# Kernel tuning notes

Hardware: AMD Instinct MI355X
Metric: run time of the kernel (lower is better)

Reference implementation:

```python
import jax, jax.numpy as jnp
import numpy as np

SEQ_LEN = 4096
D_IN = 2048
D_OUT = 2048
DROPOUT_P = 0.5


def setup_inputs() -> dict:
    key = jax.random.key(0)
    kx, kq, kk, kv = jax.random.split(key, 4)
    return {
        "x": jax.random.normal(kx, (SEQ_LEN, D_IN), dtype=jnp.float32),
        "W_query": jax.random.uniform(kq, (D_IN, D_OUT), dtype=jnp.float32),
        "W_key": jax.random.uniform(kk, (D_IN, D_OUT), dtype=jnp.float32),
        "W_value": jax.random.uniform(kv, (D_IN, D_OUT), dtype=jnp.float32),
    }


def reference(x, W_query, W_key, W_value):
    # projections: [S, d_in] @ [d_in, d_out] -> [S, d_out]
    queries = x @ W_query
    keys = x @ W_key
    values = x @ W_value
    # full score matrix [S, S]
    attn_scores = queries @ keys.T
    S = attn_scores.shape[0]
    causal_mask = jnp.triu(jnp.ones((S, S), dtype=bool), k=1)
    masked = jnp.where(causal_mask, -jnp.inf, attn_scores)
    scale = jnp.sqrt(jnp.asarray(keys.shape[-1], dtype=masked.dtype))
    attn_weights = jax.nn.softmax(masked / scale, axis=1)
    # dropout p=0.5 (train mode), inverted scaling, deterministic key
    keep = jax.random.bernoulli(jax.random.key(42), 1.0 - DROPOUT_P, attn_weights.shape)
    attn_weights = jnp.where(keep, attn_weights / (1.0 - DROPOUT_P), 0.0)
    context_vec = attn_weights @ values  # [S, d_out]
    return context_vec
```

## Files before the change

kernel.cpp:

```cpp
#include <hip/hip_runtime.h>
#include <cstdint>
#include <cstddef>
#include <cmath>

#define SEQ 4096
#define DM  2048

typedef unsigned int u32;
typedef unsigned short u16;
typedef __attribute__((ext_vector_type(8))) short bf16x8;
typedef __attribute__((ext_vector_type(4))) float f32x4;

__device__ __forceinline__ u16 f2bf(float f) {
  u32 u = __float_as_uint(f);
  return (u16)((u + 0x7FFFu + ((u >> 16) & 1u)) >> 16);
}
__device__ __forceinline__ float bf2f(u16 h) { return __uint_as_float(((u32)h) << 16); }

__device__ __forceinline__ u32 rotl32(u32 x, int r) { return (x << r) | (x >> (32 - r)); }

__device__ __forceinline__ void tf2x32(u32 c0, u32 c1, u32& o0, u32& o1) {
  const u32 k0 = 0u, k1 = 42u, k2 = 0x1BD11BDAu ^ 0u ^ 42u;
  u32 x0 = c0 + k0;
  u32 x1 = c1 + k1;
#define TFR(r) { x0 += x1; x1 = rotl32(x1, (r)); x1 ^= x0; }
  TFR(13) TFR(15) TFR(26) TFR(6)   x0 += k1; x1 += k2 + 1u;
  TFR(17) TFR(29) TFR(16) TFR(24)  x0 += k2; x1 += k0 + 2u;
  TFR(13) TFR(15) TFR(26) TFR(6)   x0 += k0; x1 += k1 + 3u;
  TFR(17) TFR(29) TFR(16) TFR(24)  x0 += k1; x1 += k2 + 4u;
  TFR(13) TFR(15) TFR(26) TFR(6)   x0 += k2; x1 += k0 + 5u;
#undef TFR
  o0 = x0; o1 = x1;
}

__device__ __forceinline__ bool dropout_keep(u32 idx) {
  u32 a, b; tf2x32(0u, idx, a, b);
  return (((a ^ b) & 0x80000000u) == 0u);
}

__device__ __forceinline__ void g2l16(const void* g, void* l) {
  __builtin_amdgcn_global_load_lds((const __attribute__((address_space(1))) u32*)g,
                                   (__attribute__((address_space(3))) u32*)l, 16, 0, 0);
}

#define MFMA16(a, b, c) __builtin_amdgcn_mfma_f32_16x16x32_bf16(a, b, c, 0, 0, 0)

template <bool SPLIT>
__device__ __forceinline__ void gemm_core(
    const u16* __restrict__ Ah, const u16* __restrict__ Al,
    const u16* __restrict__ Bh, const u16* __restrict__ Bl,
    int lda, int ldb, int rowBlock, int colBlock, int kmax,
    f32x4 (&acc)[4][4])
{
  __shared__ __align__(16) u16 Als[SPLIT ? 2 : 1][128 * 32];
  __shared__ __align__(16) u16 Bls[SPLIT ? 2 : 1][128 * 32];
  const int tid  = threadIdx.x;
  const int wid  = tid >> 6;
  const int lane = tid & 63;
  const int wr   = (wid & 1) << 6;
  const int wc   = (wid >> 1) << 6;
  const int lrow = lane & 15;
  const int lk   = (((lane >> 4) ^ ((lrow >> 1) & 3)) << 3);
  const int srow = wid * 32 + (lane >> 2);
  const int skol = (((lane & 3) ^ ((lane >> 3) & 3)) << 3);

  const f32x4 zero = {0.f, 0.f, 0.f, 0.f};
#pragma unroll
  for (int i = 0; i < 4; ++i)
#pragma unroll
    for (int j = 0; j < 4; ++j) acc[i][j] = zero;

  for (int kb = 0; kb < kmax; kb += 32) {
#pragma unroll
    for (int t = 0; t < 2; ++t) {
      const size_t ga = (size_t)(rowBlock + srow + t * 16) * lda + kb + skol;
      const size_t gb = (size_t)(colBlock + srow + t * 16) * ldb + kb + skol;
      const int lo = (wid * 32 + t * 16) * 32;
      g2l16(Ah + ga, &Als[0][lo]);
      g2l16(Bh + gb, &Bls[0][lo]);
      if constexpr (SPLIT) {
        g2l16(Al + ga, &Als[1][lo]);
        g2l16(Bl + gb, &Bls[1][lo]);
      }
    }
    __syncthreads();

    bf16x8 ah[4], bh[4], al[4], bl[4];
#pragma unroll
    for (int r = 0; r < 4; ++r) {
      ah[r] = *(const bf16x8*)&Als[0][(wr + r * 16 + lrow) * 32 + lk];
      bh[r] = *(const bf16x8*)&Bls[0][(wc + r * 16 + lrow) * 32 + lk];
      if constexpr (SPLIT) {
        al[r] = *(const bf16x8*)&Als[1][(wr + r * 16 + lrow) * 32 + lk];
        bl[r] = *(const bf16x8*)&Bls[1][(wc + r * 16 + lrow) * 32 + lk];
      }
    }
#pragma unroll
    for (int r = 0; r < 4; ++r)
#pragma unroll
      for (int c = 0; c < 4; ++c) {
        acc[r][c] = MFMA16(ah[r], bh[c], acc[r][c]);
        if constexpr (SPLIT) {
          acc[r][c] = MFMA16(ah[r], bl[c], acc[r][c]);
          acc[r][c] = MFMA16(al[r], bh[c], acc[r][c]);
        }
      }
    __syncthreads();
  }
}

__global__ __launch_bounds__(256) void k_split_x(const float* __restrict__ X,
                                                 u16* __restrict__ Xh, u16* __restrict__ Xl) {
  const size_t i = ((size_t)blockIdx.x * 256 + threadIdx.x) * 4;
  const float4 v = *(const float4*)(X + i);
  ushort4 h, l;
  h.x = f2bf(v.x); l.x = f2bf(v.x - bf2f(h.x));
  h.y = f2bf(v.y); l.y = f2bf(v.y - bf2f(h.y));
  h.z = f2bf(v.z); l.z = f2bf(v.z - bf2f(h.z));
  h.w = f2bf(v.w); l.w = f2bf(v.w - bf2f(h.w));
  *(ushort4*)(Xh + i) = h;
  *(ushort4*)(Xl + i) = l;
}

__global__ __launch_bounds__(256) void k_split_w(
    const float* __restrict__ Wq, const float* __restrict__ Wk, const float* __restrict__ Wv,
    u16* __restrict__ Wqh, u16* __restrict__ Wql,
    u16* __restrict__ Wkh, u16* __restrict__ Wkl, u16* __restrict__ Wvh) {
  const int z = blockIdx.z;
  const float* W = (z == 0) ? Wq : (z == 1) ? Wk : Wv;
  u16* Oh = (z == 0) ? Wqh : (z == 1) ? Wkh : Wvh;
  u16* Ol = (z == 0) ? Wql : Wkl;
  __shared__ float t[32][33];
  const int tx = threadIdx.x & 31, ty = threadIdx.x >> 5;
  const int n0 = blockIdx.x * 32, k0 = blockIdx.y * 32;
#pragma unroll
  for (int i = 0; i < 4; ++i)
    t[ty + i * 8][tx] = W[(size_t)(k0 + ty + i * 8) * DM + n0 + tx];
  __syncthreads();
#pragma unroll
  for (int i = 0; i < 4; ++i) {
    const int n = ty + i * 8;
    const float v = t[tx][n];
    const u16 h = f2bf(v);
    const size_t off = (size_t)(n0 + n) * DM + k0 + tx;
    Oh[off] = h;
    if (z < 2) Ol[off] = f2bf(v - bf2f(h));
  }
}

__global__ __launch_bounds__(256) void k_proj_qk(
    const u16* __restrict__ Xh, const u16* __restrict__ Xl,
    const u16* __restrict__ Wqh, const u16* __restrict__ Wql,
    const u16* __restrict__ Wkh, const u16* __restrict__ Wkl,
    u16* __restrict__ Qh, u16* __restrict__ Ql,
    u16* __restrict__ Kh, u16* __restrict__ Kl, float rscaleQ)
{
  const int z = blockIdx.z;
  const u16* Bh = z ? Wkh : Wqh;
  const u16* Bl = z ? Wkl : Wql;
  u16* Oh = z ? Kh : Qh;
  u16* Ol = z ? Kl : Ql;
  const float rs = z ? 1.0f : rscaleQ;
  f32x4 acc[4][4];
  gemm_core<true>(Xh, Xl, Bh, Bl, DM, DM, blockIdx.y * 128, blockIdx.x * 128, DM, acc);

  const int lane = threadIdx.x & 63, wid = threadIdx.x >> 6;
  const int r0 = blockIdx.y * 128 + ((wid & 1) << 6) + ((lane >> 4) << 2);
  const int c0 = blockIdx.x * 128 + ((wid >> 1) << 6) + (lane & 15);
#pragma unroll
  for (int r = 0; r < 4; ++r)
#pragma unroll
    for (int c = 0; c < 4; ++c) {
      const int col = c0 + c * 16;
#pragma unroll
      for (int e = 0; e < 4; ++e) {
        const float v = acc[r][c][e] * rs;
        const u16 h = f2bf(v);
        const size_t off = (size_t)(r0 + r * 16 + e) * DM + col;
        Oh[off] = h;
        Ol[off] = f2bf(v - bf2f(h));
      }
    }
}

__global__ __launch_bounds__(256) void k_proj_v(
    const u16* __restrict__ Xh, const u16* __restrict__ Wvh, u16* __restrict__ Vt)
{
  f32x4 acc[4][4];
  gemm_core<false>(Xh, nullptr, Wvh, nullptr, DM, DM, blockIdx.y * 128, blockIdx.x * 128, DM, acc);

  const int lane = threadIdx.x & 63, wid = threadIdx.x >> 6;
  const int r0 = blockIdx.y * 128 + ((wid & 1) << 6) + ((lane >> 4) << 2);
  const int c0 = blockIdx.x * 128 + ((wid >> 1) << 6) + (lane & 15);
#pragma unroll
  for (int r = 0; r < 4; ++r)
#pragma unroll
    for (int c = 0; c < 4; ++c) {
      const int d = c0 + c * 16;
      const int s0 = r0 + r * 16;
      ushort4 pk;
      pk.x = f2bf(acc[r][c][0]); pk.y = f2bf(acc[r][c][1]);
      pk.z = f2bf(acc[r][c][2]); pk.w = f2bf(acc[r][c][3]);
      *(ushort4*)(Vt + (size_t)d * SEQ + s0) = pk;
    }
}

__global__ __launch_bounds__(256) void k_scores(
    const u16* __restrict__ Qh, const u16* __restrict__ Ql,
    const u16* __restrict__ Kh, const u16* __restrict__ Kl, float* __restrict__ S)
{
  const int bid = blockIdx.x;
  int by = (int)((sqrtf(8.0f * (float)bid + 1.0f) - 1.0f) * 0.5f);
  while ((by + 1) * (by + 2) / 2 <= bid) ++by;
  while (by * (by + 1) / 2 > bid) --by;
  const int bx = bid - by * (by + 1) / 2;

  f32x4 acc[4][4];
  gemm_core<true>(Qh, Ql, Kh, Kl, DM, DM, by * 128, bx * 128, DM, acc);

  const int lane = threadIdx.x & 63, wid = threadIdx.x >> 6;
  const int r0 = by * 128 + ((wid & 1) << 6) + ((lane >> 4) << 2);
  const int c0 = bx * 128 + ((wid >> 1) << 6) + (lane & 15);
#pragma unroll
  for (int r = 0; r < 4; ++r)
#pragma unroll
    for (int c = 0; c < 4; ++c)
#pragma unroll
      for (int e = 0; e < 4; ++e)
        S[(size_t)(r0 + r * 16 + e) * SEQ + (c0 + c * 16)] = acc[r][c][e];
}

__global__ __launch_bounds__(256) void k_softmax_dropout(const float* __restrict__ S,
                                                         u16* __restrict__ P) {
  const int row = blockIdx.x;
  const int n = row + 1;
  const int nt = (n + 1023) >> 10;
  const int tid = threadIdx.x;
  __shared__ float buf[SEQ];
  __shared__ float red[4];
  __shared__ float bcast;
  const float* srow = S + (size_t)row * SEQ;

  float lmax = -INFINITY;
  for (int t = 0; t < nt; ++t) {
    int j4 = tid + t * 256;
    float4 v = *(const float4*)(srow + (size_t)j4 * 4);
    int b = j4 * 4;
    float x0 = (b + 0 < n) ? v.x : -INFINITY;
    float x1 = (b + 1 < n) ? v.y : -INFINITY;
    float x2 = (b + 2 < n) ? v.z : -INFINITY;
    float x3 = (b + 3 < n) ? v.w : -INFINITY;
    buf[b + 0] = x0; buf[b + 1] = x1; buf[b + 2] = x2; buf[b + 3] = x3;
    lmax = fmaxf(lmax, fmaxf(fmaxf(x0, x1), fmaxf(x2, x3)));
  }
  for (int off = 32; off > 0; off >>= 1) lmax = fmaxf(lmax, __shfl_down(lmax, off, 64));
  if ((tid & 63) == 0) red[tid >> 6] = lmax;
  __syncthreads();
  if (tid == 0) bcast = fmaxf(fmaxf(red[0], red[1]), fmaxf(red[2], red[3]));
  __syncthreads();
  const float m = bcast;

  float lsum = 0.f;
  for (int t = 0; t < nt; ++t) {
    int b = (tid + t * 256) * 4;
    float e0 = expf(buf[b + 0] - m);
    float e1 = expf(buf[b + 1] - m);
    float e2 = expf(buf[b + 2] - m);
    float e3 = expf(buf[b + 3] - m);
    buf[b + 0] = e0; buf[b + 1] = e1; buf[b + 2] = e2; buf[b + 3] = e3;
    lsum += (e0 + e1) + (e2 + e3);
  }
  for (int off = 32; off > 0; off >>= 1) lsum += __shfl_down(lsum, off, 64);
  if ((tid & 63) == 0) red[tid >> 6] = lsum;
  __syncthreads();
  if (tid == 0) bcast = (red[0] + red[1]) + (red[2] + red[3]);
  __syncthreads();
  const float total = bcast;

  u16* prow = P + (size_t)row * SEQ;
  const int zeroEnd = ((row >> 7) + 1) << 7;
  for (int j = tid; j < zeroEnd; j += 256) {
    float out = 0.f;
    if (j < n) {
      const float w = buf[j] / total;
      out = dropout_keep((u32)(row * SEQ + j)) ? w * 2.0f : 0.f;
    }
    prow[j] = f2bf(out);
  }
}

__global__ __launch_bounds__(256) void k_pv(const u16* __restrict__ P,
                                            const u16* __restrict__ Vt,
                                            float* __restrict__ O) {
  const int by = (SEQ / 128 - 1) - blockIdx.y;
  f32x4 acc[4][4];
  gemm_core<false>(P, nullptr, Vt, nullptr, SEQ, SEQ, by * 128, blockIdx.x * 128,
                   (by + 1) * 128, acc);

  const int lane = threadIdx.x & 63, wid = threadIdx.x >> 6;
  const int r0 = by * 128 + ((wid & 1) << 6) + ((lane >> 4) << 2);
  const int c0 = blockIdx.x * 128 + ((wid >> 1) << 6) + (lane & 15);
#pragma unroll
  for (int r = 0; r < 4; ++r)
#pragma unroll
    for (int c = 0; c < 4; ++c)
#pragma unroll
      for (int e = 0; e < 4; ++e)
        O[(size_t)(r0 + r * 16 + e) * DM + (c0 + c * 16)] = acc[r][c][e];
}

extern "C" void kernel_launch(void* const* d_in, const int* in_sizes, int n_in,
                              void* d_out, int out_size, void* d_ws, size_t ws_size,
                              hipStream_t stream) {
  const float* x  = (const float*)d_in[0];
  const float* Wq = (const float*)d_in[1];
  const float* Wk = (const float*)d_in[2];
  const float* Wv = (const float*)d_in[3];

  const size_t PL = (size_t)SEQ * DM;
  const size_t WL = (size_t)DM * DM;
  u16* base = (u16*)d_ws;
  u16* Qh = base;
  u16* Ql = Qh + PL;
  u16* Kh = Ql + PL;
  u16* Kl = Kh + PL;
  u16* Vt = Kl + PL;
  u16* P  = base;
  u16* regA = Vt + PL;
  u16* Xh  = regA;
  u16* Xl  = Xh + PL;
  u16* Wqh = Xl + PL;
  u16* Wql = Wqh + WL;
  u16* Wkh = Wql + WL;
  u16* Wkl = Wkh + WL;
  u16* Wvh = Wkl + WL;
  float* S = (float*)regA;

  const float rscale = 1.0f / sqrtf(2048.0f);
  dim3 blk(256);
  k_split_x<<<dim3((unsigned)(PL / 1024)), blk, 0, stream>>>(x, Xh, Xl);
  k_split_w<<<dim3(DM / 32, DM / 32, 3), blk, 0, stream>>>(Wq, Wk, Wv, Wqh, Wql, Wkh, Wkl, Wvh);
  k_proj_qk<<<dim3(DM / 128, SEQ / 128, 2), blk, 0, stream>>>(Xh, Xl, Wqh, Wql, Wkh, Wkl,
                                                              Qh, Ql, Kh, Kl, rscale);
  k_proj_v<<<dim3(DM / 128, SEQ / 128), blk, 0, stream>>>(Xh, Wvh, Vt);
  k_scores<<<dim3((SEQ / 128) * (SEQ / 128 + 1) / 2), blk, 0, stream>>>(Qh, Ql, Kh, Kl, S);
  k_softmax_dropout<<<dim3(SEQ), blk, 0, stream>>>(S, P);
  k_pv<<<dim3(DM / 128, SEQ / 128), blk, 0, stream>>>(P, Vt, (float*)d_out);
}
```

Baseline: 661.3 us.

## Store low bf16 halves in MFMA fragment order and load directly to registers

The low-order bf16 residual planes (Xl, Wql/Wkl, Ql/Kl) are now written in a pre-tiled per-lane fragment layout, so the split GEMM loads them straight from global memory into registers instead of staging them through LDS. This halves LDS traffic and shared memory per block in the Q/K projection and score GEMMs, which may raise occupancy. The split kernels and the QK projection epilogue are rewritten to emit this layout, with the epilogue using shared memory for the reshuffle. The cost is extra global loads issued before the barrier and more complex epilogues.

After: 681.5 us. +3.1%, slower.

```diff
diff --git a/kernel.cpp b/kernel.cpp
--- a/kernel.cpp
+++ b/kernel.cpp
@@ -45,15 +45,15 @@
 
 #define MFMA16(a, b, c) __builtin_amdgcn_mfma_f32_16x16x32_bf16(a, b, c, 0, 0, 0)
 
-template <bool SPLIT>
-__device__ __forceinline__ void gemm_core(
-    const u16* __restrict__ Ah, const u16* __restrict__ Al,
-    const u16* __restrict__ Bh, const u16* __restrict__ Bl,
+
+__device__ __forceinline__ void gemm_core_split(
+    const u16* __restrict__ Ah, const u16* __restrict__ AlFT,
+    const u16* __restrict__ Bh, const u16* __restrict__ BlFT,
     int lda, int ldb, int rowBlock, int colBlock, int kmax,
-    f32x4 (&acc)[4][4])
+    f32x4 (&acc)[4][4], u16* smem)
 {
-  __shared__ __align__(16) u16 Als[SPLIT ? 2 : 1][128 * 32];
-  __shared__ __align__(16) u16 Bls[SPLIT ? 2 : 1][128 * 32];
+  u16* Als = smem;
+  u16* Bls = smem + 4096;
   const int tid  = threadIdx.x;
   const int wid  = tid >> 6;
   const int lane = tid & 63;
@@ -63,6 +63,9 @@
   const int lk   = (((lane >> 4) ^ ((lrow >> 1) & 3)) << 3);
   const int srow = wid * 32 + (lane >> 2);
   const int skol = (((lane & 3) ^ ((lane >> 3) & 3)) << 3);
+  const int KA32 = lda >> 5, KB32 = ldb >> 5;
+  const int rtA = (rowBlock >> 4) + ((wid & 1) << 2);
+  const int rtB = (colBlock >> 4) + ((wid >> 1) << 2);
 
   const f32x4 zero = {0.f, 0.f, 0.f, 0.f};
 #pragma unroll
@@ -71,55 +74,113 @@
     for (int j = 0; j < 4; ++j) acc[i][j] = zero;
 
   for (int kb = 0; kb < kmax; kb += 32) {
+    const int kt = kb >> 5;
+    bf16x8 al[4], bl[4];
+#pragma unroll
+    for (int r = 0; r < 4; ++r) {
+      al[r] = *(const bf16x8*)(AlFT + (((size_t)(rtA + r) * KA32 + kt) * 64 + lane) * 8);
+      bl[r] = *(const bf16x8*)(BlFT + (((size_t)(rtB + r) * KB32 + kt) * 64 + lane) * 8);
+    }
 #pragma unroll
     for (int t = 0; t < 2; ++t) {
       const size_t ga = (size_t)(rowBlock + srow + t * 16) * lda + kb + skol;
       const size_t gb = (size_t)(colBlock + srow + t * 16) * ldb + kb + skol;
       const int lo = (wid * 32 + t * 16) * 32;
-      g2l16(Ah + ga, &Als[0][lo]);
-      g2l16(Bh + gb, &Bls[0][lo]);
-      if constexpr (SPLIT) {
-        g2l16(Al + ga, &Als[1][lo]);
-        g2l16(Bl + gb, &Bls[1][lo]);
-      }
+      g2l16(Ah + ga, &Als[lo]);
+      g2l16(Bh + gb, &Bls[lo]);
     }
     __syncthreads();
 
-    bf16x8 ah[4], bh[4], al[4], bl[4];
+    bf16x8 ah[4], bh[4];
 #pragma unroll
     for (int r = 0; r < 4; ++r) {
-      ah[r] = *(const bf16x8*)&Als[0][(wr + r * 16 + lrow) * 32 + lk];
-      bh[r] = *(const bf16x8*)&Bls[0][(wc + r * 16 + lrow) * 32 + lk];
-      if constexpr (SPLIT) {
-        al[r] = *(const bf16x8*)&Als[1][(wr + r * 16 + lrow) * 32 + lk];
-        bl[r] = *(const bf16x8*)&Bls[1][(wc + r * 16 + lrow) * 32 + lk];
-      }
+      ah[r] = *(const bf16x8*)&Als[(wr + r * 16 + lrow) * 32 + lk];
+      bh[r] = *(const bf16x8*)&Bls[(wc + r * 16 + lrow) * 32 + lk];
     }
 #pragma unroll
     for (int r = 0; r < 4; ++r)
 #pragma unroll
       for (int c = 0; c < 4; ++c) {
         acc[r][c] = MFMA16(ah[r], bh[c], acc[r][c]);
-        if constexpr (SPLIT) {
-          acc[r][c] = MFMA16(ah[r], bl[c], acc[r][c]);
-          acc[r][c] = MFMA16(al[r], bh[c], acc[r][c]);
-        }
+        acc[r][c] = MFMA16(ah[r], bl[c], acc[r][c]);
+        acc[r][c] = MFMA16(al[r], bh[c], acc[r][c]);
       }
     __syncthreads();
   }
 }
 
+__device__ __forceinline__ void gemm_core(
+    const u16* __restrict__ Ah, const u16* __restrict__ Bh,
+    int lda, int ldb, int rowBlock, int colBlock, int kmax,
+    f32x4 (&acc)[4][4])
+{
+  __shared__ __align__(16) u16 Als[128 * 32];
+  __shared__ __align__(16) u16 Bls[128 * 32];
+  const int tid  = threadIdx.x;
+  const int wid  = tid >> 6;
+  const int lane = tid & 63;
+  const int wr   = (wid & 1) << 6;
+  const int wc   = (wid >> 1) << 6;
+  const int lrow = lane & 15;
+  const int lk   = (((lane >> 4) ^ ((lrow >> 1) & 3)) << 3);
+  const int srow = wid * 32 + (lane >> 2);
+  const int skol = (((lane & 3) ^ ((lane >> 3) & 3)) << 3);
+
+  const f32x4 zero = {0.f, 0.f, 0.f, 0.f};
+#pragma unroll
+  for (int i = 0; i < 4; ++i)
+#pragma unroll
+    for (int j = 0; j < 4; ++j) acc[i][j] = zero;
+
+  for (int kb = 0; kb < kmax; kb += 32) {
+#pragma unroll
+    for (int t = 0; t < 2; ++t) {
+      const size_t ga = (size_t)(rowBlock + srow + t * 16) * lda + kb + skol;
+      const size_t gb = (size_t)(colBlock + srow + t * 16) * ldb + kb + skol;
+      const int lo = (wid * 32 + t * 16) * 32;
+      g2l16(Ah + ga, &Als[lo]);
+      g2l16(Bh + gb, &Bls[lo]);
+    }
+    __syncthreads();
+
+    bf16x8 ah[4], bh[4];
+#pragma unroll
+    for (int r = 0; r < 4; ++r) {
+      ah[r] = *(const bf16x8*)&Als[(wr + r * 16 + lrow) * 32 + lk];
+      bh[r] = *(const bf16x8*)&Bls[(wc + r * 16 + lrow) * 32 + lk];
+    }
+#pragma unroll
+    for (int r = 0; r < 4; ++r)
+#pragma unroll
+      for (int c = 0; c < 4; ++c)
+        acc[r][c] = MFMA16(ah[r], bh[c], acc[r][c]);
+    __syncthreads();
+  }
+}
+
 __global__ __launch_bounds__(256) void k_split_x(const float* __restrict__ X,
                                                  u16* __restrict__ Xh, u16* __restrict__ Xl) {
-  const size_t i = ((size_t)blockIdx.x * 256 + threadIdx.x) * 4;
-  const float4 v = *(const float4*)(X + i);
-  ushort4 h, l;
-  h.x = f2bf(v.x); l.x = f2bf(v.x - bf2f(h.x));
-  h.y = f2bf(v.y); l.y = f2bf(v.y - bf2f(h.y));
-  h.z = f2bf(v.z); l.z = f2bf(v.z - bf2f(h.z));
-  h.w = f2bf(v.w); l.w = f2bf(v.w - bf2f(h.w));
-  *(ushort4*)(Xh + i) = h;
-  *(ushort4*)(Xl + i) = l;
+  const int wid = threadIdx.x >> 6, lane = threadIdx.x & 63;
+  const int kt = blockIdx.x;
+  const int rt = blockIdx.y * 4 + wid;
+  const int row = rt * 16 + (lane & 15);
+  const int col = kt * 32 + ((lane >> 4) << 3);
+  const float* src = X + (size_t)row * DM + col;
+  const float4 v0 = *(const float4*)src;
+  const float4 v1 = *(const float4*)(src + 4);
+  float v[8] = {v0.x, v0.y, v0.z, v0.w, v1.x, v1.y, v1.z, v1.w};
+  u16 h[8], l[8];
+#pragma unroll
+  for (int j = 0; j < 8; ++j) {
+    h[j] = f2bf(v[j]);
+    l[j] = f2bf(v[j] - bf2f(h[j]));
+  }
+  u16* hp = Xh + (size_t)row * DM + col;
+  *(ushort4*)hp = *(ushort4*)&h[0];
+  *(ushort4*)(hp + 4) = *(ushort4*)&h[4];
+  u16* lp = Xl + (((size_t)rt * 64 + kt) * 64 + lane) * 8;
+  *(ushort4*)lp = *(ushort4*)&l[0];
+  *(ushort4*)(lp + 4) = *(ushort4*)&l[4];
 }
 
 __global__ __launch_bounds__(256) void k_split_w(
@@ -130,21 +191,40 @@
   const float* W = (z == 0) ? Wq : (z == 1) ? Wk : Wv;
   u16* Oh = (z == 0) ? Wqh : (z == 1) ? Wkh : Wvh;
   u16* Ol = (z == 0) ? Wql : Wkl;
-  __shared__ float t[32][33];
-  const int tx = threadIdx.x & 31, ty = threadIdx.x >> 5;
-  const int n0 = blockIdx.x * 32, k0 = blockIdx.y * 32;
-#pragma unroll
-  for (int i = 0; i < 4; ++i)
-    t[ty + i * 8][tx] = W[(size_t)(k0 + ty + i * 8) * DM + n0 + tx];
-  __syncthreads();
-#pragma unroll
-  for (int i = 0; i < 4; ++i) {
-    const int n = ty + i * 8;
-    const float v = t[tx][n];
-    const u16 h = f2bf(v);
-    const size_t off = (size_t)(n0 + n) * DM + k0 + tx;
-    Oh[off] = h;
-    if (z < 2) Ol[off] = f2bf(v - bf2f(h));
+  __shared__ float t[64][65];
+  const int tid = threadIdx.x;
+  const int n0 = blockIdx.x * 64, k0 = blockIdx.y * 64;
+  const int tx = tid & 63, ty = tid >> 6;
+#pragma unroll
+  for (int i = 0; i < 16; ++i)
+    t[ty * 16 + i][tx] = W[(size_t)(k0 + ty * 16 + i) * DM + n0 + tx];
+  __syncthreads();
+  {
+    const int nl = tid >> 2, kc = (tid & 3) * 16;
+    u16 h[16];
+#pragma unroll
+    for (int i = 0; i < 16; ++i) h[i] = f2bf(t[kc + i][nl]);
+    u16* hp = Oh + (size_t)(n0 + nl) * DM + k0 + kc;
+#pragma unroll
+    for (int i = 0; i < 4; ++i) *(ushort4*)(hp + i * 4) = *(ushort4*)&h[i * 4];
+  }
+  if (z < 2) {
+    const int wid = tid >> 6, lane = tid & 63;
+#pragma unroll
+    for (int kt = 0; kt < 2; ++kt) {
+      const int nl = wid * 16 + (lane & 15);
+      const int kc = kt * 32 + ((lane >> 4) << 3);
+      u16 l[8];
+#pragma unroll
+      for (int j = 0; j < 8; ++j) {
+        const float v = t[kc + j][nl];
+        l[j] = f2bf(v - bf2f(f2bf(v)));
+      }
+      const int rtg = (n0 >> 4) + wid, ktg = (k0 >> 5) + kt;
+      u16* lp = Ol + (((size_t)rtg * 64 + ktg) * 64 + lane) * 8;
+      *(ushort4*)lp = *(ushort4*)&l[0];
+      *(ushort4*)(lp + 4) = *(ushort4*)&l[4];
+    }
   }
 }
 
@@ -155,39 +235,53 @@
     u16* __restrict__ Qh, u16* __restrict__ Ql,
     u16* __restrict__ Kh, u16* __restrict__ Kl, float rscaleQ)
 {
+  __shared__ __align__(16) u16 smem[128 * 128];
   const int z = blockIdx.z;
   const u16* Bh = z ? Wkh : Wqh;
   const u16* Bl = z ? Wkl : Wql;
   u16* Oh = z ? Kh : Qh;
   u16* Ol = z ? Kl : Ql;
   const float rs = z ? 1.0f : rscaleQ;
+  const int rowBlock = blockIdx.y * 128, colBlock = blockIdx.x * 128;
   f32x4 acc[4][4];
-  gemm_core<true>(Xh, Xl, Bh, Bl, DM, DM, blockIdx.y * 128, blockIdx.x * 128, DM, acc);
+  gemm_core_split(Xh, Xl, Bh, Bl, DM, DM, rowBlock, colBlock, DM, acc, smem);
 
   const int lane = threadIdx.x & 63, wid = threadIdx.x >> 6;
-  const int r0 = blockIdx.y * 128 + ((wid & 1) << 6) + ((lane >> 4) << 2);
-  const int c0 = blockIdx.x * 128 + ((wid >> 1) << 6) + (lane & 15);
+  const int lr0 = ((wid & 1) << 6) + ((lane >> 4) << 2);
+  const int lc0 = ((wid >> 1) << 6) + (lane & 15);
 #pragma unroll
   for (int r = 0; r < 4; ++r)
 #pragma unroll
-    for (int c = 0; c < 4; ++c) {
-      const int col = c0 + c * 16;
+    for (int c = 0; c < 4; ++c)
 #pragma unroll
       for (int e = 0; e < 4; ++e) {
         const float v = acc[r][c][e] * rs;
         const u16 h = f2bf(v);
-        const size_t off = (size_t)(r0 + r * 16 + e) * DM + col;
-        Oh[off] = h;
-        Ol[off] = f2bf(v - bf2f(h));
+        const int lrow = lr0 + r * 16 + e, lcol = lc0 + c * 16;
+        Oh[(size_t)(rowBlock + lrow) * DM + colBlock + lcol] = h;
+        smem[lrow * 128 + lcol] = f2bf(v - bf2f(h));
       }
-    }
+  __syncthreads();
+#pragma unroll
+  for (int t8 = 0; t8 < 8; ++t8) {
+    const int idx = wid * 8 + t8;
+    const int rt = idx >> 2, kt = idx & 3;
+    u16 l[8];
+#pragma unroll
+    for (int j = 0; j < 8; ++j)
+      l[j] = smem[(rt * 16 + (lane & 15)) * 128 + kt * 32 + ((lane >> 4) << 3) + j];
+    const int rtg = (rowBlock >> 4) + rt, ktg = (colBlock >> 5) + kt;
+    u16* lp = Ol + (((size_t)rtg * (DM / 32) + ktg) * 64 + lane) * 8;
+    *(ushort4*)lp = *(ushort4*)&l[0];
+    *(ushort4*)(lp + 4) = *(ushort4*)&l[4];
+  }
 }
 
 __global__ __launch_bounds__(256) void k_proj_v(
     const u16* __restrict__ Xh, const u16* __restrict__ Wvh, u16* __restrict__ Vt)
 {
   f32x4 acc[4][4];
-  gemm_core<false>(Xh, nullptr, Wvh, nullptr, DM, DM, blockIdx.y * 128, blockIdx.x * 128, DM, acc);
+  gemm_core(Xh, Wvh, DM, DM, blockIdx.y * 128, blockIdx.x * 128, DM, acc);
 
   const int lane = threadIdx.x & 63, wid = threadIdx.x >> 6;
   const int r0 = blockIdx.y * 128 + ((wid & 1) << 6) + ((lane >> 4) << 2);
@@ -209,6 +303,7 @@
     const u16* __restrict__ Qh, const u16* __restrict__ Ql,
     const u16* __restrict__ Kh, const u16* __restrict__ Kl, float* __restrict__ S)
 {
+  __shared__ __align__(16) u16 smem[128 * 64];
   const int bid = blockIdx.x;
   int by = (int)((sqrtf(8.0f * (float)bid + 1.0f) - 1.0f) * 0.5f);
   while ((by + 1) * (by + 2) / 2 <= bid) ++by;
@@ -216,7 +311,7 @@
   const int bx = bid - by * (by + 1) / 2;
 
   f32x4 acc[4][4];
-  gemm_core<true>(Qh, Ql, Kh, Kl, DM, DM, by * 128, bx * 128, DM, acc);
+  gemm_core_split(Qh, Ql, Kh, Kl, DM, DM, by * 128, bx * 128, DM, acc, smem);
 
   const int lane = threadIdx.x & 63, wid = threadIdx.x >> 6;
   const int r0 = by * 128 + ((wid & 1) << 6) + ((lane >> 4) << 2);
@@ -294,8 +389,7 @@
                                             float* __restrict__ O) {
   const int by = (SEQ / 128 - 1) - blockIdx.y;
   f32x4 acc[4][4];
-  gemm_core<false>(P, nullptr, Vt, nullptr, SEQ, SEQ, by * 128, blockIdx.x * 128,
-                   (by + 1) * 128, acc);
+  gemm_core(P, Vt, SEQ, SEQ, by * 128, blockIdx.x * 128, (by + 1) * 128, acc);
 
   const int lane = threadIdx.x & 63, wid = threadIdx.x >> 6;
   const int r0 = by * 128 + ((wid & 1) << 6) + ((lane >> 4) << 2);
@@ -338,8 +432,8 @@
 
   const float rscale = 1.0f / sqrtf(2048.0f);
   dim3 blk(256);
-  k_split_x<<<dim3((unsigned)(PL / 1024)), blk, 0, stream>>>(x, Xh, Xl);
-  k_split_w<<<dim3(DM / 32, DM / 32, 3), blk, 0, stream>>>(Wq, Wk, Wv, Wqh, Wql, Wkh, Wkl, Wvh);
+  k_split_x<<<dim3(DM / 32, SEQ / 64), blk, 0, stream>>>(x, Xh, Xl);
+  k_split_w<<<dim3(DM / 64, DM / 64, 3), blk, 0, stream>>>(Wq, Wk, Wv, Wqh, Wql, Wkh, Wkl, Wvh);
   k_proj_qk<<<dim3(DM / 128, SEQ / 128, 2), blk, 0, stream>>>(Xh, Xl, Wqh, Wql, Wkh, Wkl,
                                                               Qh, Ql, Kh, Kl, rscale);
   k_proj_v<<<dim3(DM / 128, SEQ / 128), blk, 0, stream>>>(Xh, Wvh, Vt);
```
